# Performance work log

Measured on AMD Instinct MI355X. Metric: run time of the kernel, lower is better.

Reference implementation:

```python
import jax, jax.numpy as jnp
import numpy as np

W0 = 30.0  # Sine frequency


def _bilinear_sample(plane, gx, gy):
    """torch.grid_sample(mode='bilinear', padding_mode='zeros', align_corners=True).
    plane: (C,H,W); gx,gy: (P,) normalized coords in [-1,1]. Returns (P,C)."""
    C, H, W = plane.shape
    ix = (gx + 1.0) * 0.5 * (W - 1)
    iy = (gy + 1.0) * 0.5 * (H - 1)
    x0 = jnp.floor(ix); y0 = jnp.floor(iy)
    x1 = x0 + 1.0;      y1 = y0 + 1.0
    wx1 = ix - x0; wx0 = 1.0 - wx1
    wy1 = iy - y0; wy0 = 1.0 - wy1

    def corner(xc, yc, w):
        valid = ((xc >= 0) & (xc <= W - 1) & (yc >= 0) & (yc <= H - 1)).astype(plane.dtype)
        xi = jnp.clip(xc, 0, W - 1).astype(jnp.int32)
        yi = jnp.clip(yc, 0, H - 1).astype(jnp.int32)
        return plane[:, yi, xi] * (w * valid)  # (C,P)

    out = (corner(x0, y0, wx0 * wy0) + corner(x1, y0, wx1 * wy0)
           + corner(x0, y1, wx0 * wy1) + corner(x1, y1, wx1 * wy1))
    return out.T  # (P,C)


def setup_inputs() -> dict:
    key = jax.random.key(0)
    ks = jax.random.split(key, 8)
    N = 500_000
    C, H, W = 128, 256, 256
    coords = jax.random.uniform(ks[0], (1, N, 3), jnp.float32, minval=-1.0, maxval=1.0)
    planes = [jax.random.normal(ks[1 + i], (1, C, H, W), jnp.float32) * 0.1 for i in range(3)]
    # Linear weights: first layer sine init, then frequency_init(30) for layers 2,3
    W1 = jax.random.uniform(ks[4], (C, C), jnp.float32, minval=-1.0 / C, maxval=1.0 / C)
    lim = np.sqrt(6.0 / C) / W0
    W2 = jax.random.uniform(ks[5], (C, C), jnp.float32, minval=-lim, maxval=lim)
    W3 = jax.random.uniform(ks[6], (1, C), jnp.float32, minval=-lim, maxval=lim)
    return {
        "coordinates": coords,
        "plane_xy": planes[0], "plane_yz": planes[1], "plane_xz": planes[2],
        "W1": W1, "b1": jnp.zeros((C,), jnp.float32),
        "W2": W2, "b2": jnp.zeros((C,), jnp.float32),
        "W3": W3, "b3": jnp.zeros((1,), jnp.float32),
    }


def reference(coordinates, plane_xy, plane_yz, plane_xz, W1, b1, W2, b2, W3, b3):
    B, N, _ = coordinates.shape  # B must be 1 (plane batch is 1, as in torch)
    c = coordinates.reshape(-1, 3)
    p0 = plane_xy[0]
    # NOTE: original module samples the *xz* coords from embeddings[0] (plane_xy) —
    # a bug we faithfully preserve — and multiplies [xy, xz, xz]; yz_embed is unused.
    xy = _bilinear_sample(p0, c[:, 0], c[:, 1])  # (P,C)
    xz = _bilinear_sample(p0, c[:, 0], c[:, 2])  # (P,C)
    features = xy * xz * xz
    h = jnp.sin(W0 * (features @ W1.T + b1))
    h = jnp.sin(W0 * (h @ W2.T + b2))
    out = h @ W3.T + b3
    return out.reshape(B, N, 1)
```

## Files before the change

kernel.cpp:

```cpp
#include <hip/hip_runtime.h>
#include <hip/hip_fp16.h>

typedef float f32x4 __attribute__((ext_vector_type(4)));
typedef _Float16 f16x8 __attribute__((ext_vector_type(8)));

#define CDIM 128
#define HW 256

__global__ __launch_bounds__(256) void k_transpose(const float* __restrict__ plane,
                                                   unsigned short* __restrict__ planeT) {
    __shared__ unsigned short tile[32][130];
    int tid = threadIdx.x;
    int y  = blockIdx.x >> 3;
    int x0 = (blockIdx.x & 7) * 32;
    int tx = tid & 31, tc = tid >> 5;
    for (int cc = 0; cc < 128; cc += 8) {
        int c = cc + tc;
        float v = plane[c * (HW * HW) + y * HW + x0 + tx];
        tile[tx][c] = __half_as_ushort(__float2half(v));
    }
    __syncthreads();
    for (int it = 0; it < 16; ++it) {
        int idx = it * 256 + tid;
        int c = idx & 127, xi = idx >> 7;
        planeT[(y * HW + x0 + xi) * CDIM + c] = tile[xi][c];
    }
}

__global__ __launch_bounds__(256) void k_wconv(const float* __restrict__ W1,
                                               const float* __restrict__ W2,
                                               unsigned short* __restrict__ W1h,
                                               unsigned short* __restrict__ W2h) {
    int i = blockIdx.x * 256 + threadIdx.x;
    if (i < 16384) W1h[i] = __half_as_ushort(__float2half(W1[i]));
    else           W2h[i - 16384] = __half_as_ushort(__float2half(W2[i - 16384]));
}

struct PrepT {
    int off[8];
    __half2 w[4];
    __half2 v[4];
};

__device__ __forceinline__ PrepT prep(const float* __restrict__ coords, int p, int cg) {
    PrepT r;
    float gx = coords[p * 3 + 0];
    float gy = coords[p * 3 + 1];
    float gz = coords[p * 3 + 2];
    float ix = (gx + 1.f) * 127.5f;
    float iy = (gy + 1.f) * 127.5f;
    float iz = (gz + 1.f) * 127.5f;
    float xf = floorf(ix), yf = floorf(iy), zf = floorf(iz);
    float wx1 = ix - xf, wy1 = iy - yf, wz1 = iz - zf;
    float wx0 = 1.f - wx1, wy0 = 1.f - wy1, wz0 = 1.f - wz1;
    int x0 = max(0, min((int)xf, HW - 1));
    int y0 = max(0, min((int)yf, HW - 1));
    int z0 = max(0, min((int)zf, HW - 1));
    int x1 = min(x0 + 1, HW - 1);
    int y1 = min(y0 + 1, HW - 1);
    int z1 = min(z0 + 1, HW - 1);
    int cx0 = x0 * CDIM + cg * 8, cx1 = x1 * CDIM + cg * 8;
    r.off[0] = (y0 << 15) + cx0; r.off[1] = (y0 << 15) + cx1;
    r.off[2] = (y1 << 15) + cx0; r.off[3] = (y1 << 15) + cx1;
    r.off[4] = (z0 << 15) + cx0; r.off[5] = (z0 << 15) + cx1;
    r.off[6] = (z1 << 15) + cx0; r.off[7] = (z1 << 15) + cx1;
    r.w[0] = __float2half2_rn(wy0 * wx0);
    r.w[1] = __float2half2_rn(wy0 * wx1);
    r.w[2] = __float2half2_rn(wy1 * wx0);
    r.w[3] = __float2half2_rn(wy1 * wx1);
    r.v[0] = __float2half2_rn(wz0 * wx0);
    r.v[1] = __float2half2_rn(wz0 * wx1);
    r.v[2] = __float2half2_rn(wz1 * wx0);
    r.v[3] = __float2half2_rn(wz1 * wx1);
    return r;
}

struct LdT { uint4 d[8]; };

__device__ __forceinline__ LdT ld8(const unsigned short* __restrict__ planeT, const PrepT& a) {
    LdT r;
#pragma unroll
    for (int c = 0; c < 8; ++c)
        r.d[c] = *reinterpret_cast<const uint4*>(planeT + a.off[c]);
    return r;
}

__device__ __forceinline__ __half2 geth2(const uint4& u, int g) {
    const unsigned* p = reinterpret_cast<const unsigned*>(&u);
    return __builtin_bit_cast(__half2, p[g]);
}

__device__ __forceinline__ void interp_store(unsigned short* dst, const PrepT& a, const LdT& L) {
    unsigned o[4];
#pragma unroll
    for (int g = 0; g < 4; ++g) {
        __half2 xy = __hmul2(a.w[0], geth2(L.d[0], g));
        xy = __hfma2(a.w[1], geth2(L.d[1], g), xy);
        xy = __hfma2(a.w[2], geth2(L.d[2], g), xy);
        xy = __hfma2(a.w[3], geth2(L.d[3], g), xy);
        __half2 xz = __hmul2(a.v[0], geth2(L.d[4], g));
        xz = __hfma2(a.v[1], geth2(L.d[5], g), xz);
        xz = __hfma2(a.v[2], geth2(L.d[6], g), xz);
        xz = __hfma2(a.v[3], geth2(L.d[7], g), xz);
        __half2 f = __hmul2(xy, __hmul2(xz, xz));
        o[g] = __builtin_bit_cast(unsigned, f);
    }
    uint4 pack; pack.x = o[0]; pack.y = o[1]; pack.z = o[2]; pack.w = o[3];
    *reinterpret_cast<uint4*>(dst) = pack;
}

__global__ __launch_bounds__(256, 2) void k_all(const float* __restrict__ coords,
                                                const unsigned short* __restrict__ planeT,
                                                const unsigned short* __restrict__ W1h,
                                                const unsigned short* __restrict__ W2h,
                                                const float* __restrict__ b1,
                                                const float* __restrict__ b2,
                                                const float* __restrict__ W3,
                                                const float* __restrict__ b3,
                                                float* __restrict__ out, int N) {
    __shared__ alignas(16) uint4 W1L[128][16];
    __shared__ alignas(16) uint4 W2L[128][16];
    __shared__ alignas(16) unsigned short featS[64][128];

    const int tid  = threadIdx.x;
    const int wave = tid >> 6, lane = tid & 63;
    const int ro   = wave * 16;
    const int j = lane & 15, rg = lane >> 4;
    const int pt = lane >> 4, cg = lane & 15;

#pragma unroll
    for (int i = 0; i < 8; ++i) {
        int idx = i * 256 + tid;
        int row = idx >> 4, col = idx & 15;
        W1L[row][col ^ (row & 15)] = reinterpret_cast<const uint4*>(W1h)[idx];
        W2L[row][col ^ (row & 15)] = reinterpret_cast<const uint4*>(W2h)[idx];
    }
    float b1v[8], b2v[8], w3v[8];
#pragma unroll
    for (int nt = 0; nt < 8; ++nt) {
        b1v[nt] = b1[nt * 16 + j];
        b2v[nt] = b2[nt * 16 + j];
        w3v[nt] = W3[nt * 16 + j];
    }
    const float bb3 = b3[0];
    __syncthreads();

    const int ntiles = (N + 63) >> 6;
    for (int t = blockIdx.x; t < ntiles; t += gridDim.x) {
        const int pbase = t * 64 + ro;

        {
            PrepT a0 = prep(coords, min(pbase + 0 * 4 + pt, N - 1), cg);
            LdT   d0 = ld8(planeT, a0);
            PrepT a1 = prep(coords, min(pbase + 1 * 4 + pt, N - 1), cg);
            LdT   d1 = ld8(planeT, a1);
            PrepT a2 = prep(coords, min(pbase + 2 * 4 + pt, N - 1), cg);
            LdT   d2 = ld8(planeT, a2);
            PrepT a3 = prep(coords, min(pbase + 3 * 4 + pt, N - 1), cg);
            LdT   d3 = ld8(planeT, a3);
            interp_store(&featS[ro + 0 * 4 + pt][(cg ^ (0 * 4 + pt)) * 8], a0, d0);
            interp_store(&featS[ro + 1 * 4 + pt][(cg ^ (1 * 4 + pt)) * 8], a1, d1);
            interp_store(&featS[ro + 2 * 4 + pt][(cg ^ (2 * 4 + pt)) * 8], a2, d2);
            interp_store(&featS[ro + 3 * 4 + pt][(cg ^ (3 * 4 + pt)) * 8], a3, d3);
        }

        __syncthreads();

        f32x4 acc[8];
#pragma unroll
        for (int nt = 0; nt < 8; ++nt) acc[nt] = (f32x4){0.f, 0.f, 0.f, 0.f};

        f16x8 af[4];
#pragma unroll
        for (int kk = 0; kk < 4; ++kk)
            af[kk] = __builtin_bit_cast(f16x8, *reinterpret_cast<const uint4*>(&featS[ro + j][((kk * 4 + rg) ^ j) * 8]));

#pragma unroll
        for (int kk = 0; kk < 4; ++kk) {
            f16x8 bf[8];
#pragma unroll
            for (int nt = 0; nt < 8; ++nt)
                bf[nt] = __builtin_bit_cast(f16x8, W1L[nt * 16 + j][(kk * 4 + rg) ^ j]);
#pragma unroll
            for (int nt = 0; nt < 8; ++nt)
                acc[nt] = __builtin_amdgcn_mfma_f32_16x16x32_f16(af[kk], bf[nt], acc[nt], 0, 0, 0);
        }

#pragma unroll
        for (int nt = 0; nt < 8; ++nt) {
#pragma unroll
            for (int r = 0; r < 4; ++r) {
                float h = __sinf(30.f * (acc[nt][r] + b1v[nt]));
                int row = rg * 4 + r;
                int g = (nt * 2 + (j >> 3)) ^ row;
                featS[ro + row][g * 8 + (j & 7)] = __half_as_ushort(__float2half(h));
            }
        }

        __syncthreads();

        f32x4 acc2[8];
#pragma unroll
        for (int nt = 0; nt < 8; ++nt) acc2[nt] = (f32x4){0.f, 0.f, 0.f, 0.f};

        f16x8 af2[4];
#pragma unroll
        for (int kk = 0; kk < 4; ++kk)
            af2[kk] = __builtin_bit_cast(f16x8, *reinterpret_cast<const uint4*>(&featS[ro + j][((kk * 4 + rg) ^ j) * 8]));

#pragma unroll
        for (int kk = 0; kk < 4; ++kk) {
            f16x8 bf[8];
#pragma unroll
            for (int nt = 0; nt < 8; ++nt)
                bf[nt] = __builtin_bit_cast(f16x8, W2L[nt * 16 + j][(kk * 4 + rg) ^ j]);
#pragma unroll
            for (int nt = 0; nt < 8; ++nt)
                acc2[nt] = __builtin_amdgcn_mfma_f32_16x16x32_f16(af2[kk], bf[nt], acc2[nt], 0, 0, 0);
        }

        float part[4] = {0.f, 0.f, 0.f, 0.f};
#pragma unroll
        for (int nt = 0; nt < 8; ++nt) {
#pragma unroll
            for (int r = 0; r < 4; ++r)
                part[r] += __sinf(30.f * (acc2[nt][r] + b2v[nt])) * w3v[nt];
        }
#pragma unroll
        for (int off = 1; off < 16; off <<= 1) {
#pragma unroll
            for (int r = 0; r < 4; ++r) part[r] += __shfl_xor(part[r], off, 64);
        }
        if (j == 0) {
#pragma unroll
            for (int r = 0; r < 4; ++r) {
                int p = pbase + rg * 4 + r;
                if (p < N) out[p] = part[r] + bb3;
            }
        }

        __syncthreads();
    }
}

extern "C" void kernel_launch(void* const* d_in, const int* in_sizes, int n_in,
                              void* d_out, int out_size, void* d_ws, size_t ws_size,
                              hipStream_t stream) {
    const float* coords = (const float*)d_in[0];
    const float* plane  = (const float*)d_in[1];
    const float* W1     = (const float*)d_in[4];
    const float* b1     = (const float*)d_in[5];
    const float* W2     = (const float*)d_in[6];
    const float* b2     = (const float*)d_in[7];
    const float* W3     = (const float*)d_in[8];
    const float* b3     = (const float*)d_in[9];
    float* out = (float*)d_out;
    int N = in_sizes[0] / 3;

    char* ws = (char*)d_ws;
    unsigned short* planeT = (unsigned short*)ws;
    unsigned short* W1h = (unsigned short*)(ws + 16777216);
    unsigned short* W2h = (unsigned short*)(ws + 16809984);

    k_transpose<<<dim3(HW * 8), dim3(256), 0, stream>>>(plane, planeT);
    k_wconv<<<dim3(128), dim3(256), 0, stream>>>(W1, W2, W1h, W2h);

    k_all<<<dim3(512), dim3(256), 0, stream>>>(coords, planeT, W1h, W2h,
                                               b1, b2, W3, b3, out, N);
    (void)ws_size;
}
```

Measured before the change: 125.9 us.

## Bin points by x-cell and map bins to XCDs for plane gather locality

```diff
diff --git a/kernel.cpp b/kernel.cpp
--- a/kernel.cpp
+++ b/kernel.cpp
@@ -6,6 +6,11 @@
 
 #define CDIM 128
 #define HW 256
+#define NBINS 256
+#define BINCAP 2560
+#define TILES_PER_BIN 40
+#define BINS_PER_XCD 32
+#define GRID_MAIN 512
 
 __global__ __launch_bounds__(256) void k_transpose(const float* __restrict__ plane,
                                                    unsigned short* __restrict__ planeT) {
@@ -36,17 +41,56 @@
     else           W2h[i - 16384] = __half_as_ushort(__float2half(W2[i - 16384]));
 }
 
+__global__ __launch_bounds__(256) void k_scatter(const float* __restrict__ coords,
+                                                 float4* __restrict__ bins,
+                                                 int* __restrict__ cursor, int N) {
+    __shared__ int hist[NBINS];
+    __shared__ int rnk[NBINS];
+    __shared__ int base[NBINS];
+    const int tid = threadIdx.x;
+    hist[tid] = 0; rnk[tid] = 0;
+    __syncthreads();
+
+    const int start = blockIdx.x * 2048;
+    float gx[8], gy[8], gz[8]; int bn[8];
+#pragma unroll
+    for (int k = 0; k < 8; ++k) {
+        int p = start + k * 256 + tid;
+        if (p < N) {
+            gx[k] = coords[p * 3 + 0];
+            gy[k] = coords[p * 3 + 1];
+            gz[k] = coords[p * 3 + 2];
+            float ix = (gx[k] + 1.f) * 127.5f;
+            bn[k] = max(0, min((int)floorf(ix), HW - 1));
+            atomicAdd(&hist[bn[k]], 1);
+        } else bn[k] = -1;
+    }
+    __syncthreads();
+    if (hist[tid] > 0) base[tid] = atomicAdd(&cursor[tid], hist[tid]);
+    __syncthreads();
+#pragma unroll
+    for (int k = 0; k < 8; ++k) {
+        if (bn[k] >= 0) {
+            int p = start + k * 256 + tid;
+            int r = atomicAdd(&rnk[bn[k]], 1);
+            int pos = base[bn[k]] + r;
+            if (pos < BINCAP) {
+                float4 rec; rec.x = gx[k]; rec.y = gy[k]; rec.z = gz[k];
+                rec.w = __int_as_float(p);
+                bins[(size_t)bn[k] * BINCAP + pos] = rec;
+            }
+        }
+    }
+}
+
 struct PrepT {
     int off[8];
     __half2 w[4];
     __half2 v[4];
 };
 
-__device__ __forceinline__ PrepT prep(const float* __restrict__ coords, int p, int cg) {
+__device__ __forceinline__ PrepT prepV(float gx, float gy, float gz, int cg) {
     PrepT r;
-    float gx = coords[p * 3 + 0];
-    float gy = coords[p * 3 + 1];
-    float gz = coords[p * 3 + 2];
     float ix = (gx + 1.f) * 127.5f;
     float iy = (gy + 1.f) * 127.5f;
     float iz = (gz + 1.f) * 127.5f;
@@ -109,7 +153,10 @@
     *reinterpret_cast<uint4*>(dst) = pack;
 }
 
+template <bool SORTED>
 __global__ __launch_bounds__(256, 2) void k_all(const float* __restrict__ coords,
+                                                const float4* __restrict__ bins,
+                                                const int* __restrict__ cursor,
                                                 const unsigned short* __restrict__ planeT,
                                                 const unsigned short* __restrict__ W1h,
                                                 const unsigned short* __restrict__ W2h,
@@ -145,19 +192,43 @@
     const float bb3 = b3[0];
     __syncthreads();
 
-    const int ntiles = (N + 63) >> 6;
-    for (int t = blockIdx.x; t < ntiles; t += gridDim.x) {
-        const int pbase = t * 64 + ro;
+    const int ntt = SORTED ? (NBINS * TILES_PER_BIN) : ((N + 63) >> 6);
+    for (int tt = blockIdx.x; tt < ntt; tt += gridDim.x) {
+        int bin = 0, base = 0, cnt = 0, pbase = 0;
+        if (SORTED) {
+            int xcd = tt & 7, jj = tt >> 3;
+            bin  = xcd * BINS_PER_XCD + jj / TILES_PER_BIN;
+            base = (jj % TILES_PER_BIN) * 64;
+            cnt  = min(cursor[bin], BINCAP);
+            if (base >= cnt) continue;
+        } else {
+            pbase = tt * 64 + ro;
+        }
+        const float4* brec = bins + (size_t)bin * BINCAP;
 
         {
-            PrepT a0 = prep(coords, min(pbase + 0 * 4 + pt, N - 1), cg);
-            LdT   d0 = ld8(planeT, a0);
-            PrepT a1 = prep(coords, min(pbase + 1 * 4 + pt, N - 1), cg);
-            LdT   d1 = ld8(planeT, a1);
-            PrepT a2 = prep(coords, min(pbase + 2 * 4 + pt, N - 1), cg);
-            LdT   d2 = ld8(planeT, a2);
-            PrepT a3 = prep(coords, min(pbase + 3 * 4 + pt, N - 1), cg);
-            LdT   d3 = ld8(planeT, a3);
+            PrepT a0, a1, a2, a3;
+#pragma unroll
+            for (int it = 0; it < 4; ++it) {
+                float gx, gy, gz;
+                if (SORTED) {
+                    int q = min(base + ro + it * 4 + pt, cnt - 1);
+                    float4 s = brec[q];
+                    gx = s.x; gy = s.y; gz = s.z;
+                } else {
+                    int p = min(pbase + it * 4 + pt, N - 1);
+                    gx = coords[p * 3 + 0];
+                    gy = coords[p * 3 + 1];
+                    gz = coords[p * 3 + 2];
+                }
+                PrepT a = prepV(gx, gy, gz, cg);
+                if (it == 0) a0 = a; else if (it == 1) a1 = a;
+                else if (it == 2) a2 = a; else a3 = a;
+            }
+            LdT d0 = ld8(planeT, a0);
+            LdT d1 = ld8(planeT, a1);
+            LdT d2 = ld8(planeT, a2);
+            LdT d3 = ld8(planeT, a3);
             interp_store(&featS[ro + 0 * 4 + pt][(cg ^ (0 * 4 + pt)) * 8], a0, d0);
             interp_store(&featS[ro + 1 * 4 + pt][(cg ^ (1 * 4 + pt)) * 8], a1, d1);
             interp_store(&featS[ro + 2 * 4 + pt][(cg ^ (2 * 4 + pt)) * 8], a2, d2);
@@ -234,8 +305,16 @@
         if (j == 0) {
 #pragma unroll
             for (int r = 0; r < 4; ++r) {
-                int p = pbase + rg * 4 + r;
-                if (p < N) out[p] = part[r] + bb3;
+                int pl = rg * 4 + r;
+                if (SORTED) {
+                    if (base + ro + pl < cnt) {
+                        int orig = __float_as_int(brec[base + ro + pl].w);
+                        out[orig] = part[r] + bb3;
+                    }
+                } else {
+                    int p = pbase + pl;
+                    if (p < N) out[p] = part[r] + bb3;
+                }
             }
         }
 
@@ -261,11 +340,20 @@
     unsigned short* planeT = (unsigned short*)ws;
     unsigned short* W1h = (unsigned short*)(ws + 16777216);
     unsigned short* W2h = (unsigned short*)(ws + 16809984);
+    int*    cursor = (int*)(ws + 16842752);
+    float4* bins   = (float4*)(ws + 16843776);
+    const size_t need = 16843776 + (size_t)NBINS * BINCAP * 16;
 
     k_transpose<<<dim3(HW * 8), dim3(256), 0, stream>>>(plane, planeT);
     k_wconv<<<dim3(128), dim3(256), 0, stream>>>(W1, W2, W1h, W2h);
 
-    k_all<<<dim3(512), dim3(256), 0, stream>>>(coords, planeT, W1h, W2h,
-                                               b1, b2, W3, b3, out, N);
-    (void)ws_size;
-}
+    if (ws_size >= need) {
+        hipMemsetAsync(cursor, 0, NBINS * sizeof(int), stream);
+        k_scatter<<<dim3((N + 2047) / 2048), dim3(256), 0, stream>>>(coords, bins, cursor, N);
+        k_all<true><<<dim3(GRID_MAIN), dim3(256), 0, stream>>>(
+            coords, bins, cursor, planeT, W1h, W2h, b1, b2, W3, b3, out, N);
+    } else {
+        k_all<false><<<dim3(GRID_MAIN), dim3(256), 0, stream>>>(
+            coords, bins, cursor, planeT, W1h, W2h, b1, b2, W3, b3, out, N);
+    }
+}
```

After: 129.3 us. 2.7% more time.
